# Optimization experiments

Measured on AMD Instinct MI355X. Metric: run time of the kernel, lower is better.

Reference implementation:

```python
import jax, jax.numpy as jnp
import numpy as np

# dims
N, D, H = 10000, 512, 8            # nodes, node hidden, heads
E, EL, M = 120000, 60000, 600000   # graph edges, local edges, line-graph edges
ED, EH = 64, 8                     # edge feat dim (relation_share_heads), edge heads
L, R = 4, 100                      # gnn layers, relation vocab
DK, EDK = D // H, ED // EH
SCALE_N, SCALE_E = float(np.sqrt(DK)), float(np.sqrt(EDK))


def layer_norm(h, g, b, eps=1e-5):
    mu = jnp.mean(h, axis=-1, keepdims=True)
    var = jnp.mean((h - mu) ** 2, axis=-1, keepdims=True)
    return (h - mu) * jax.lax.rsqrt(var + eps) * g + b


def setup_inputs() -> dict:
    key = jax.random.key(0)
    ks = iter(jax.random.split(key, 80))

    def nrm(shape, s=0.02):
        return jax.random.normal(next(ks), shape, jnp.float32) * s

    inp = {
        "x": jax.random.normal(next(ks), (N, D), jnp.float32),
        "rel_embed": nrm((R, ED), 1.0),
        # node-update (RAT) params, stacked over layers
        "Wq": nrm((L, D, D)), "bq": jnp.zeros((L, D), jnp.float32),
        "Wk": nrm((L, D, D)), "Wv": nrm((L, D, D)),
        "Wo": nrm((L, D, D)), "bo": jnp.zeros((L, D), jnp.float32),
        "ln1_g": jnp.ones((L, D), jnp.float32), "ln1_b": jnp.zeros((L, D), jnp.float32),
        "F1": nrm((L, D, 4 * D)), "f1b": jnp.zeros((L, 4 * D), jnp.float32),
        "F2": nrm((L, 4 * D, D)), "f2b": jnp.zeros((L, D), jnp.float32),
        "ln2_g": jnp.ones((L, D), jnp.float32), "ln2_b": jnp.zeros((L, D), jnp.float32),
        # edge-update (metapath line-graph attention) params
        "Eq": nrm((L, ED, ED)), "eqb": jnp.zeros((L, ED), jnp.float32),
        "Ek": nrm((L, ED, ED)), "Ev": nrm((L, ED, ED)),
        "Eo": nrm((L, ED, ED)), "eob": jnp.zeros((L, ED), jnp.float32),
        "Ns": nrm((L, D, ED)), "nsb": jnp.zeros((L, ED), jnp.float32),
        "Nd": nrm((L, D, ED)), "ndb": jnp.zeros((L, ED), jnp.float32),
        "eln1_g": jnp.ones((L, ED), jnp.float32), "eln1_b": jnp.zeros((L, ED), jnp.float32),
        "G1": nrm((L, ED, 4 * ED)), "g1b": jnp.zeros((L, 4 * ED), jnp.float32),
        "G2": nrm((L, 4 * ED, ED)), "g2b": jnp.zeros((L, ED), jnp.float32),
        "eln2_g": jnp.ones((L, ED), jnp.float32), "eln2_b": jnp.zeros((L, ED), jnp.float32),
        # graph structure (constants)
        "edge_feat": jax.random.randint(next(ks), (E,), 0, R),
        "local_index": jnp.arange(EL),
        "src_ids": jax.random.randint(next(ks), (EL,), 0, N),
        "dst_ids": jax.random.randint(next(ks), (EL,), 0, N),
        "g_src": jax.random.randint(next(ks), (E,), 0, N),
        "g_dst": jax.random.randint(next(ks), (E,), 0, N),
        "lg_src": jax.random.randint(next(ks), (M,), 0, EL),
        "lg_dst": jax.random.randint(next(ks), (M,), 0, EL),
    }
    return inp


def reference(x, rel_embed, Wq, bq, Wk, Wv, Wo, bo, ln1_g, ln1_b, F1, f1b, F2, f2b,
              ln2_g, ln2_b, Eq, eqb, Ek, Ev, Eo, eob, Ns, nsb, Nd, ndb,
              eln1_g, eln1_b, G1, g1b, G2, g2b, eln2_g, eln2_b,
              edge_feat, local_index, src_ids, dst_ids, g_src, g_dst, lg_src, lg_dst):
    lg_x = rel_embed[edge_feat]        # [E, ED] relation embedding gather
    lg_x_local = lg_x[local_index]     # [EL, ED]
    for i in range(L):
        x_in = x
        # ---- node update: relation-aware multi-head attention over g ----
        q = (x_in @ Wq[i] + bq[i]).reshape(N, H, DK)
        k = (x_in @ Wk[i]).reshape(N, H, DK)
        v = (x_in @ Wv[i]).reshape(N, H, DK)
        e = lg_x[:, None, :]           # relation feat shared across heads (edim == d_k)
        ks = k[g_src] + e              # [E, H, DK]
        vs = v[g_src] + e
        s = jnp.einsum('ehd,ehd->eh', ks, q[g_dst]) / SCALE_N
        w = jnp.exp(jnp.clip(s, -10.0, 10.0))
        wv = jax.ops.segment_sum(w[..., None] * vs, g_dst, num_segments=N)
        z = jax.ops.segment_sum(w, g_dst, num_segments=N)
        o = (wv / jnp.maximum(z, 1e-9)[..., None]).reshape(N, D)
        h = layer_norm(x_in + o @ Wo[i] + bo[i], ln1_g[i], ln1_b[i])
        x = layer_norm(h + jax.nn.relu(h @ F1[i] + f1b[i]) @ F2[i] + f2b[i], ln2_g[i], ln2_b[i])
        # ---- edge update: attention over line graph lg, metapath = shared node feat ----
        src_x = x_in[src_ids]          # index_select on pre-update x
        dst_x = x_in[dst_ids]
        qe = (lg_x_local @ Eq[i] + eqb[i] + src_x @ Ns[i] + nsb[i]).reshape(EL, EH, EDK)
        me = (dst_x @ Nd[i] + ndb[i]).reshape(EL, EH, EDK)
        ke = (lg_x_local @ Ek[i]).reshape(EL, EH, EDK) + me
        ve = (lg_x_local @ Ev[i]).reshape(EL, EH, EDK) + me
        se = jnp.einsum('mhd,mhd->mh', ke[lg_src], qe[lg_dst]) / SCALE_E
        we = jnp.exp(jnp.clip(se, -10.0, 10.0))
        wve = jax.ops.segment_sum(we[..., None] * ve[lg_src], lg_dst, num_segments=EL)
        ze = jax.ops.segment_sum(we, lg_dst, num_segments=EL)
        oe = (wve / jnp.maximum(ze, 1e-9)[..., None]).reshape(EL, ED)
        he = layer_norm(lg_x_local + oe @ Eo[i] + eob[i], eln1_g[i], eln1_b[i])
        out_local = layer_norm(he + jax.nn.relu(he @ G1[i] + g1b[i]) @ G2[i] + g2b[i],
                               eln2_g[i], eln2_b[i])
        lg_x = lg_x.at[local_index].set(out_local)   # masked_scatter_
        lg_x_local = out_local
    return (x, lg_x_local)
```

## Files before the change

### kernel.cpp

```cpp
#include <hip/hip_runtime.h>
#include <math.h>

#define NN   10000
#define DD   512
#define NH   8
#define NE   120000
#define NEL  60000
#define NLG  600000
#define ED   64
#define NEH  8
#define NL   4
#define QKVW 1536

typedef __attribute__((ext_vector_type(8))) short bf16x8;
typedef __attribute__((ext_vector_type(8))) unsigned short u16x8;
typedef __attribute__((ext_vector_type(4))) float f32x4;

__device__ __forceinline__ unsigned short f2b(float f) {
    union { float f; unsigned u; } c; c.f = f;
    unsigned u = c.u;
    unsigned r = u + 0x7FFFu + ((u >> 16) & 1u);
    return (unsigned short)(r >> 16);
}
__device__ __forceinline__ float b2f(unsigned short b) {
    union { unsigned u; float f; } c; c.u = ((unsigned)b) << 16;
    return c.f;
}

__device__ __forceinline__ void gl16(const unsigned short* g, unsigned short* l) {
    __builtin_amdgcn_global_load_lds(
        (const __attribute__((address_space(1))) unsigned int*)g,
        (__attribute__((address_space(3))) unsigned int*)l, 16, 0, 0);
}

static __global__ __launch_bounds__(256)
void zero_k(float* __restrict__ p, int n) {
    int i = blockIdx.x * 256 + threadIdx.x;
    if (i < n) p[i] = 0.0f;
}

static __global__ __launch_bounds__(256)
void castcopy_k(const float* __restrict__ s, float* __restrict__ d,
                unsigned short* __restrict__ db, int n) {
    int i = blockIdx.x * 256 + threadIdx.x;
    if (i < n) { float v = s[i]; if (d) d[i] = v; db[i] = f2b(v); }
}

static __global__ __launch_bounds__(256)
void init_lg_k(const float* __restrict__ rel, const int* __restrict__ ef,
               unsigned short* __restrict__ lgb) {
    int i = blockIdx.x * 256 + threadIdx.x;
    if (i >= NE * ED) return;
    int e = i >> 6, c = i & 63;
    lgb[i] = f2b(rel[ef[e] * ED + c]);
}

static __global__ __launch_bounds__(256)
void gather64_k(const unsigned short* __restrict__ lgb, const int* __restrict__ idx,
                float* __restrict__ el, unsigned short* __restrict__ elb) {
    int i = blockIdx.x * 256 + threadIdx.x;
    if (i >= NEL * ED) return;
    int r = i >> 6;
    unsigned short b = lgb[(long)idx[r] * ED + (i & 63)];
    el[i] = b2f(b); elb[i] = b;
}

static __global__ __launch_bounds__(256)
void ttrans_k(const float* __restrict__ in, unsigned short* __restrict__ out,
              int K, int N, long lstride, int rowStride, int rowOff, int colOff) {
    __shared__ float sm[32][33];
    const int l = blockIdx.z;
    const int kt = blockIdx.x * 32, nt = blockIdx.y * 32;
    const int tx = threadIdx.x & 31, ty = threadIdx.x >> 5;
    const float* ip = in + (size_t)l * K * N;
    #pragma unroll
    for (int r = 0; r < 4; ++r)
        sm[ty + 8 * r][tx] = ip[(size_t)(kt + ty + 8 * r) * N + nt + tx];
    __syncthreads();
    unsigned short* op = out + (size_t)l * lstride;
    #pragma unroll
    for (int r = 0; r < 4; ++r) {
        int n = nt + ty + 8 * r;
        op[(size_t)(rowOff + n) * rowStride + colOff + kt + tx] = f2b(sm[tx][ty + 8 * r]);
    }
}

static __global__ __launch_bounds__(256)
void build_qkvb_k(const float* __restrict__ bq, float* __restrict__ out) {
    int i = blockIdx.x * 256 + threadIdx.x;
    if (i >= NL * QKVW) return;
    int l = i / QKVW, c = i - l * QKVW;
    out[i] = (c < 512) ? bq[l * 512 + c] : 0.0f;
}

static __global__ __launch_bounds__(256)
void ebias_k(const float* __restrict__ ndb, const float* __restrict__ eqb,
             const float* __restrict__ nsb, float* __restrict__ kvb,
             float* __restrict__ qb2) {
    int i = blockIdx.x * 256 + threadIdx.x;
    if (i < NL * 128) kvb[i] = ndb[(i >> 7) * 64 + (i & 63)];
    if (i < NL * 64)  qb2[i] = eqb[i] + nsb[i];
}

static __global__ __launch_bounds__(256)
void hist_k(const int* __restrict__ dst, int* __restrict__ cnt, int n) {
    int i = blockIdx.x * 256 + threadIdx.x;
    if (i < n) atomicAdd(&cnt[dst[i]], 1);
}

static __global__ __launch_bounds__(256)
void scanA_k(const int* __restrict__ cnt, int* __restrict__ off,
             int* __restrict__ bsum, int n) {
    __shared__ int sm[256];
    const int t = threadIdx.x;
    const int i = blockIdx.x * 256 + t;
    int v = (i < n) ? cnt[i] : 0;
    sm[t] = v; __syncthreads();
    int x = v;
    #pragma unroll
    for (int d = 1; d < 256; d <<= 1) {
        int y = (t >= d) ? sm[t - d] : 0;
        __syncthreads();
        x += y; sm[t] = x; __syncthreads();
    }
    if (i < n) off[i] = x - v;
    if (t == 255) bsum[blockIdx.x] = x;
}

static __global__ __launch_bounds__(1024)
void scanB_k(int* __restrict__ bsum, int nb) {
    __shared__ int sm[1024];
    const int t = threadIdx.x;
    int v = (t < nb) ? bsum[t] : 0;
    sm[t] = v; __syncthreads();
    int x = v;
    #pragma unroll
    for (int d = 1; d < 1024; d <<= 1) {
        int y = (t >= d) ? sm[t - d] : 0;
        __syncthreads();
        x += y; sm[t] = x; __syncthreads();
    }
    if (t < nb) bsum[t] = x - v;
}

static __global__ __launch_bounds__(256)
void scanC_k(const int* __restrict__ bsum, int* __restrict__ off,
             int* __restrict__ cur, int n) {
    int i = blockIdx.x * 256 + threadIdx.x;
    if (i < n) { int o = off[i] + bsum[blockIdx.x]; off[i] = o; cur[i] = o; }
}

static __global__ __launch_bounds__(256)
void scatter_k(const int* __restrict__ dst, int* __restrict__ cur,
               int* __restrict__ ord, int n) {
    int i = blockIdx.x * 256 + threadIdx.x;
    if (i < n) { int p = atomicAdd(&cur[dst[i]], 1); ord[p] = i; }
}

static __global__ __launch_bounds__(256)
void pack_k(const int* __restrict__ gord, const int* __restrict__ gsrc,
            const int* __restrict__ eord, const int* __restrict__ lsrc,
            int2* __restrict__ npack, int* __restrict__ esrc) {
    int i = blockIdx.x * 256 + threadIdx.x;
    if (i < NE) { int e = gord[i]; npack[i] = make_int2(e, gsrc[e]); }
    if (i < NLG) esrc[i] = lsrc[eord[i]];
}

#define FSWZ(r) (((r) & 3) ^ (((r) >> 2) & 3))
template<int BM, int BN>
static __global__ __launch_bounds__(256)
void gemm_bf16_k(const unsigned short* __restrict__ A,
                 const unsigned short* __restrict__ A2, const int* __restrict__ idx2,
                 const unsigned short* __restrict__ Bt, const float* __restrict__ bias,
                 const float* __restrict__ addC, const unsigned short* __restrict__ addCb,
                 float* __restrict__ C, unsigned short* __restrict__ Cb,
                 int M, int K, int Nc, int doRelu, int K1)
{
    constexpr int MI = BM / 32, NI = BN / 32;
    constexpr int AC = BM / 64, BC = BN / 64;
    __shared__ unsigned short Asl[BM * 32];
    __shared__ unsigned short Bsl[BN * 32];
    const int tid  = threadIdx.x;
    const int lane = tid & 63;
    const int wave = tid >> 6;
    const int wr = (wave >> 1) * (BM / 2);
    const int wc = (wave & 1) * (BN / 2);

    const int nwg = gridDim.x * gridDim.y;
    const int hw = blockIdx.y * gridDim.x + blockIdx.x;
    const int q8 = nwg >> 3, r8 = nwg & 7;
    const int xcd = hw & 7, rest = hw >> 3;
    const int logical = (xcd < r8 ? xcd * (q8 + 1) : r8 * (q8 + 1) + (xcd - r8) * q8) + rest;
    const int bm = (logical / gridDim.x) * BM;
    const int bn = (logical % gridDim.x) * BN;

    const int rl = lane >> 2;
    const int sl = lane & 3;
    int ga[AC]; long ia[AC]; bool av[AC]; int acw[AC];
    #pragma unroll
    for (int c = 0; c < AC; ++c) {
        int ar = wave * (BM / 4) + c * 16 + rl;
        ga[c] = bm + ar;
        av[c] = ga[c] < M;
        ia[c] = (A2 && av[c]) ? (long)idx2[ga[c]] : 0;
        acw[c] = (sl ^ FSWZ(ar)) * 8;
    }
    int gb[BC]; int bcw[BC];
    #pragma unroll
    for (int c = 0; c < BC; ++c) {
        int br = wave * (BN / 4) + c * 16 + rl;
        gb[c] = bn + br;
        bcw[c] = (sl ^ FSWZ(br)) * 8;
    }

    auto stage = [&](int k0) {
        #pragma unroll
        for (int c = 0; c < AC; ++c) {
            const unsigned short* s;
            if (!A2)            s = A  + (long)ga[c] * K  + k0 + acw[c];
            else if (k0 < K1)   s = A  + (long)ga[c] * K1 + k0 + acw[c];
            else                s = A2 + ia[c] * DD + (k0 - K1) + acw[c];
            if (av[c]) gl16(s, Asl + (wave * (BM / 4) + c * 16) * 32);
        }
        #pragma unroll
        for (int c = 0; c < BC; ++c)
            gl16(Bt + (long)gb[c] * K + k0 + bcw[c],
                 Bsl + (wave * (BN / 4) + c * 16) * 32);
    };

    f32x4 acc[MI][NI] = {};
    const int rbase = lane & 15;
    const int ks = lane >> 4;

    for (int k0 = 0; k0 < K; k0 += 32) {
        stage(k0);
        __syncthreads();
        bf16x8 af[MI]; bf16x8 bfr[NI];
        #pragma unroll
        for (int mi = 0; mi < MI; ++mi) {
            int r = wr + mi * 16 + rbase;
            int s = ks ^ FSWZ(r);
            af[mi] = *reinterpret_cast<const bf16x8*>(Asl + r * 32 + s * 8);
        }
        #pragma unroll
        for (int ni = 0; ni < NI; ++ni) {
            int r = wc + ni * 16 + rbase;
            int s = ks ^ FSWZ(r);
            bfr[ni] = *reinterpret_cast<const bf16x8*>(Bsl + r * 32 + s * 8);
        }
        #pragma unroll
        for (int mi = 0; mi < MI; ++mi)
            #pragma unroll
            for (int ni = 0; ni < NI; ++ni)
                acc[mi][ni] = __builtin_amdgcn_mfma_f32_16x16x32_bf16(
                    af[mi], bfr[ni], acc[mi][ni], 0, 0, 0);
        __syncthreads();
    }

    const int colBase = bn + wc + rbase;
    const int rowBase = bm + wr + ks * 4;
    #pragma unroll
    for (int mi = 0; mi < MI; ++mi) {
        #pragma unroll
        for (int j = 0; j < 4; ++j) {
            int r = rowBase + mi * 16 + j;
            if (r >= M) continue;
            long ro = (long)r * Nc;
            #pragma unroll
            for (int ni = 0; ni < NI; ++ni) {
                int cc = colBase + ni * 16;
                if (cc >= Nc) continue;
                float v = acc[mi][ni][j];
                if (bias)  v += bias[cc];
                if (doRelu) v = fmaxf(v, 0.0f);
                if (addC)  v += addC[ro + cc];
                else if (addCb) v += b2f(addCb[ro + cc]);
                if (Cb) Cb[ro + cc] = f2b(v);
                else    C[ro + cc] = v;
            }
        }
    }
}
#undef FSWZ

static __global__ __launch_bounds__(256)
void ln_k(const float* __restrict__ in, const float* __restrict__ g,
          const float* __restrict__ b, float* __restrict__ out, int Dw, int nrows,
          unsigned short* __restrict__ outb,
          unsigned short* __restrict__ out2b, const int* __restrict__ idx2)
{
    const int row = blockIdx.x * 4 + (threadIdx.x >> 6);
    if (row >= nrows) return;
    const int lane = threadIdx.x & 63;
    const int per = Dw >> 6;
    float v[8];
    const float* rp = in + (long)row * Dw;
    float s = 0.f;
    for (int i = 0; i < per; ++i) { v[i] = rp[i * 64 + lane]; s += v[i]; }
    #pragma unroll
    for (int off = 32; off; off >>= 1) s += __shfl_xor(s, off, 64);
    const float mu = s / (float)Dw;
    float var = 0.f;
    for (int i = 0; i < per; ++i) { float d = v[i] - mu; var += d * d; }
    #pragma unroll
    for (int off = 32; off; off >>= 1) var += __shfl_xor(var, off, 64);
    const float rstd = rsqrtf(var / (float)Dw + 1e-5f);
    for (int i = 0; i < per; ++i) {
        int c = i * 64 + lane;
        float o = (v[i] - mu) * rstd * g[c] + b[c];
        if (out)   out[(long)row * Dw + c] = o;
        if (outb)  outb[(long)row * Dw + c] = f2b(o);
        if (out2b) out2b[(long)idx2[row] * Dw + c] = f2b(o);
    }
}

static __global__ __launch_bounds__(256)
void node_attn_csr_k(const unsigned short* __restrict__ qkv,
                     const unsigned short* __restrict__ lgb,
                     const int* __restrict__ goff, const int2* __restrict__ npack,
                     unsigned short* __restrict__ ob)
{
    int node = blockIdx.x * 4 + (threadIdx.x >> 6);
    if (node >= NN) return;
    const int lane = threadIdx.x & 63;
    float qv[8];
    {
        u16x8 q8 = *reinterpret_cast<const u16x8*>(qkv + (long)node * QKVW + lane * 8);
        #pragma unroll
        for (int i = 0; i < 8; ++i) qv[i] = b2f(q8[i]);
    }
    float wva[8] = {0.f, 0.f, 0.f, 0.f, 0.f, 0.f, 0.f, 0.f};
    float zac = 0.f;
    int j = goff[node];
    const int hi = (node + 1 < NN) ? goff[node + 1] : NE;
    const int eoffl = (lane & 7) * 8;

    for (; j + 2 <= hi; j += 2) {
        int2 pa = npack[j], pb = npack[j + 1];
        u16x8 kA = *reinterpret_cast<const u16x8*>(qkv + (long)pa.y * QKVW + 512 + lane * 8);
        u16x8 vA = *reinterpret_cast<const u16x8*>(qkv + (long)pa.y * QKVW + 1024 + lane * 8);
        u16x8 eA = *reinterpret_cast<const u16x8*>(lgb + (long)pa.x * ED + eoffl);
        u16x8 kB = *reinterpret_cast<const u16x8*>(qkv + (long)pb.y * QKVW + 512 + lane * 8);
        u16x8 vB = *reinterpret_cast<const u16x8*>(qkv + (long)pb.y * QKVW + 1024 + lane * 8);
        u16x8 eB = *reinterpret_cast<const u16x8*>(lgb + (long)pb.x * ED + eoffl);
        float edA[8], vvA[8], edB[8], vvB[8];
        float pA = 0.f, pB = 0.f;
        #pragma unroll
        for (int i = 0; i < 8; ++i) {
            edA[i] = b2f(eA[i]); vvA[i] = b2f(vA[i]);
            pA = fmaf(b2f(kA[i]) + edA[i], qv[i], pA);
            edB[i] = b2f(eB[i]); vvB[i] = b2f(vB[i]);
            pB = fmaf(b2f(kB[i]) + edB[i], qv[i], pB);
        }
        pA += __shfl_xor(pA, 1, 64); pA += __shfl_xor(pA, 2, 64); pA += __shfl_xor(pA, 4, 64);
        pB += __shfl_xor(pB, 1, 64); pB += __shfl_xor(pB, 2, 64); pB += __shfl_xor(pB, 4, 64);
        float wA = expf(fminf(fmaxf(pA * 0.125f, -10.0f), 10.0f));
        float wB = expf(fminf(fmaxf(pB * 0.125f, -10.0f), 10.0f));
        #pragma unroll
        for (int i = 0; i < 8; ++i) {
            wva[i] = fmaf(wA, vvA[i] + edA[i], wva[i]);
            wva[i] = fmaf(wB, vvB[i] + edB[i], wva[i]);
        }
        zac += wA + wB;
    }
    for (; j < hi; ++j) {
        int2 pa = npack[j];
        u16x8 kA = *reinterpret_cast<const u16x8*>(qkv + (long)pa.y * QKVW + 512 + lane * 8);
        u16x8 vA = *reinterpret_cast<const u16x8*>(qkv + (long)pa.y * QKVW + 1024 + lane * 8);
        u16x8 eA = *reinterpret_cast<const u16x8*>(lgb + (long)pa.x * ED + eoffl);
        float edA[8], vvA[8];
        float pA = 0.f;
        #pragma unroll
        for (int i = 0; i < 8; ++i) {
            edA[i] = b2f(eA[i]); vvA[i] = b2f(vA[i]);
            pA = fmaf(b2f(kA[i]) + edA[i], qv[i], pA);
        }
        pA += __shfl_xor(pA, 1, 64); pA += __shfl_xor(pA, 2, 64); pA += __shfl_xor(pA, 4, 64);
        float wA = expf(fminf(fmaxf(pA * 0.125f, -10.0f), 10.0f));
        #pragma unroll
        for (int i = 0; i < 8; ++i) wva[i] = fmaf(wA, vvA[i] + edA[i], wva[i]);
        zac += wA;
    }
    const float inv = 1.0f / fmaxf(zac, 1e-9f);
    u16x8 o8;
    #pragma unroll
    for (int i = 0; i < 8; ++i) o8[i] = f2b(wva[i] * inv);
    *reinterpret_cast<u16x8*>(ob + (long)node * DD + lane * 8) = o8;
}

static __global__ __launch_bounds__(256)
void lg_attn_csr_k(const unsigned short* __restrict__ qeb,
                   const unsigned short* __restrict__ keve,
                   const int* __restrict__ eoff, const int* __restrict__ esrc,
                   unsigned short* __restrict__ oeb)
{
    int d = blockIdx.x * 4 + (threadIdx.x >> 6);
    if (d >= NEL) return;
    const int lane = threadIdx.x & 63;
    const float qv = b2f(qeb[(long)d * ED + lane]);
    float oa = 0.f, zac = 0.f;
    int j = eoff[d];
    const int hi = (d + 1 < NEL) ? eoff[d + 1] : NLG;
    for (; j + 4 <= hi; j += 4) {
        int ss[4]; float kk[4], vv[4];
        #pragma unroll
        for (int u = 0; u < 4; ++u) ss[u] = esrc[j + u];
        #pragma unroll
        for (int u = 0; u < 4; ++u) {
            kk[u] = b2f(keve[(long)ss[u] * 128 + lane]);
            vv[u] = b2f(keve[(long)ss[u] * 128 + 64 + lane]);
        }
        #pragma unroll
        for (int u = 0; u < 4; ++u) {
            float p = kk[u] * qv;
            p += __shfl_xor(p, 1, 64); p += __shfl_xor(p, 2, 64); p += __shfl_xor(p, 4, 64);
            float w = expf(fminf(fmaxf(p * 0.35355339059327373f, -10.0f), 10.0f));
            oa = fmaf(w, vv[u], oa);
            zac += w;
        }
    }
    for (; j < hi; ++j) {
        int s = esrc[j];
        float kv = b2f(keve[(long)s * 128 + lane]);
        float vv = b2f(keve[(long)s * 128 + 64 + lane]);
        float p = kv * qv;
        p += __shfl_xor(p, 1, 64); p += __shfl_xor(p, 2, 64); p += __shfl_xor(p, 4, 64);
        float w = expf(fminf(fmaxf(p * 0.35355339059327373f, -10.0f), 10.0f));
        oa = fmaf(w, vv, oa);
        zac += w;
    }
    oeb[(long)d * ED + lane] = f2b(oa / fmaxf(zac, 1e-9f));
}

static inline void run_gemm(hipStream_t st, const unsigned short* A,
                            const unsigned short* Bt, const float* bias,
                            const float* addC, const unsigned short* addCb,
                            float* C, unsigned short* Cb,
                            int M, int K, int Nc, int relu)
{
    dim3 g((Nc + 63) / 64, (M + 63) / 64);
    gemm_bf16_k<64, 64><<<g, 256, 0, st>>>(A, nullptr, nullptr, Bt, bias, addC, addCb,
                                           C, Cb, M, K, Nc, relu, 0);
}
static inline void run_gemm2(hipStream_t st, const unsigned short* A1,
                             const unsigned short* A2, const int* idx2,
                             const unsigned short* Bt, const float* bias,
                             unsigned short* Cb, int M, int K, int Nc, int K1)
{
    dim3 g((Nc + 63) / 64, (M + 63) / 64);
    gemm_bf16_k<64, 64><<<g, 256, 0, st>>>(A1, A2, idx2, Bt, bias, nullptr, nullptr,
                                           nullptr, Cb, M, K, Nc, 0, K1);
}

extern "C" void kernel_launch(void* const* d_in, const int* in_sizes, int n_in,
                              void* d_out, int out_size, void* d_ws, size_t ws_size,
                              hipStream_t stream)
{
    const float* x_in  = (const float*)d_in[0];
    const float* rel   = (const float*)d_in[1];
    const float* Wq    = (const float*)d_in[2];
    const float* bq    = (const float*)d_in[3];
    const float* Wk    = (const float*)d_in[4];
    const float* Wv    = (const float*)d_in[5];
    const float* Wo    = (const float*)d_in[6];
    const float* bo    = (const float*)d_in[7];
    const float* ln1g  = (const float*)d_in[8];
    const float* ln1b  = (const float*)d_in[9];
    const float* F1    = (const float*)d_in[10];
    const float* f1b   = (const float*)d_in[11];
    const float* F2    = (const float*)d_in[12];
    const float* f2b_  = (const float*)d_in[13];
    const float* ln2g  = (const float*)d_in[14];
    const float* ln2b  = (const float*)d_in[15];
    const float* Eq    = (const float*)d_in[16];
    const float* eqb   = (const float*)d_in[17];
    const float* Ek    = (const float*)d_in[18];
    const float* Ev    = (const float*)d_in[19];
    const float* Eo    = (const float*)d_in[20];
    const float* eob   = (const float*)d_in[21];
    const float* Ns    = (const float*)d_in[22];
    const float* nsb   = (const float*)d_in[23];
    const float* Nd    = (const float*)d_in[24];
    const float* ndb   = (const float*)d_in[25];
    const float* eln1g = (const float*)d_in[26];
    const float* eln1b = (const float*)d_in[27];
    const float* G1    = (const float*)d_in[28];
    const float* g1b   = (const float*)d_in[29];
    const float* G2    = (const float*)d_in[30];
    const float* g2b   = (const float*)d_in[31];
    const float* eln2g = (const float*)d_in[32];
    const float* eln2b = (const float*)d_in[33];
    const int* edge_feat   = (const int*)d_in[34];
    const int* local_index = (const int*)d_in[35];
    const int* src_ids     = (const int*)d_in[36];
    const int* dst_ids     = (const int*)d_in[37];
    const int* g_src       = (const int*)d_in[38];
    const int* g_dst       = (const int*)d_in[39];
    const int* lg_src      = (const int*)d_in[40];
    const int* lg_dst      = (const int*)d_in[41];

    float* xbuf = (float*)d_out;
    float* el   = xbuf + (size_t)NN * DD;

    float* W = (float*)d_ws;
    size_t off = 0;
    auto alloc = [&](size_t n) { float* p = W + off; off += (n + 63) & ~(size_t)63; return p; };
    float* t0  = alloc((size_t)NN * DD);
    float* t2  = alloc((size_t)NEL * ED);
    float* t3  = alloc((size_t)NEL * ED);
    float* qkvb = alloc((size_t)NL * QKVW);
    float* kvb  = alloc((size_t)NL * 128);
    float* qb2  = alloc((size_t)NL * ED);

    unsigned short* bp = (unsigned short*)(W + off);
    size_t boff = 0;
    auto balloc = [&](size_t n) { unsigned short* p = bp + boff; boff += (n + 63) & ~(size_t)63; return p; };
    unsigned short* lgb = balloc((size_t)NE * ED);
    unsigned short* xb  = balloc((size_t)NN * DD);
    unsigned short* qkv = balloc((size_t)NN * QKVW);
    unsigned short* elb = balloc((size_t)NEL * ED);
    unsigned short* e1b = balloc((size_t)NEL * ED);
    unsigned short* heb = balloc((size_t)NEL * ED);
    unsigned short* qeb = balloc((size_t)NEL * ED);
    unsigned short* fgb = balloc((size_t)NN * 4 * DD);
    unsigned short* hb   = qkv;
    unsigned short* keve = qkv + (size_t)NN * DD;
    unsigned short* ob   = fgb;
    unsigned short* WqkvT = balloc((size_t)NL * QKVW * DD);
    unsigned short* WoT  = balloc((size_t)NL * DD * DD);
    unsigned short* F1T  = balloc((size_t)NL * DD * 4 * DD);
    unsigned short* F2T  = balloc((size_t)NL * 4 * DD * DD);
    unsigned short* KVET = balloc((size_t)NL * 128 * 576);
    unsigned short* QET  = balloc((size_t)NL * 64 * 576);
    unsigned short* EoT  = balloc((size_t)NL * ED * ED);
    unsigned short* G1T  = balloc((size_t)NL * ED * 4 * ED);
    unsigned short* G2T  = balloc((size_t)NL * 4 * ED * ED);
    int* ip = (int*)(bp + ((boff + 63) & ~(size_t)63));
    size_t ioff = 0;
    auto ialloc = [&](size_t n) { int* p = ip + ioff; ioff += (n + 63) & ~(size_t)63; return p; };
    int* gcnt = ialloc(NN);
    int* goff = ialloc(NN);
    int* gcur = ialloc(NN);
    int* gord = ialloc(NE);
    int2* npack = (int2*)ialloc(2 * (size_t)NE);
    int* ecnt = ialloc(NEL);
    int* eoff = ialloc(NEL);
    int* ecur = ialloc(NEL);
    int* eord = ialloc(NLG);
    int* esrc = ialloc(NLG);
    int* bsum = ialloc(1024);

    auto tt = [&](const float* src, unsigned short* dst, int K, int N,
                  long lstride, int rowStride, int rowOff, int colOff) {
        dim3 g(K / 32, N / 32, NL);
        ttrans_k<<<g, 256, 0, stream>>>(src, dst, K, N, lstride, rowStride, rowOff, colOff);
    };
    tt(Wq, WqkvT, 512, 512, (long)QKVW * DD, DD, 0, 0);
    tt(Wk, WqkvT, 512, 512, (long)QKVW * DD, DD, 512, 0);
    tt(Wv, WqkvT, 512, 512, (long)QKVW * DD, DD, 1024, 0);
    tt(Wo, WoT, 512, 512, (long)DD * DD, DD, 0, 0);
    tt(F1, F1T, 512, 2048, (long)DD * 4 * DD, DD, 0, 0);
    tt(F2, F2T, 2048, 512, (long)4 * DD * DD, 4 * DD, 0, 0);
    tt(Ek, KVET, 64, 64, (long)128 * 576, 576, 0, 0);
    tt(Nd, KVET, 512, 64, (long)128 * 576, 576, 0, 64);
    tt(Ev, KVET, 64, 64, (long)128 * 576, 576, 64, 0);
    tt(Nd, KVET, 512, 64, (long)128 * 576, 576, 64, 64);
    tt(Eq, QET, 64, 64, (long)64 * 576, 576, 0, 0);
    tt(Ns, QET, 512, 64, (long)64 * 576, 576, 0, 64);
    tt(Eo, EoT, 64, 64, (long)ED * ED, ED, 0, 0);
    tt(G1, G1T, 64, 256, (long)ED * 4 * ED, ED, 0, 0);
    tt(G2, G2T, 256, 64, (long)4 * ED * ED, 4 * ED, 0, 0);
    build_qkvb_k<<<(NL * QKVW + 255) / 256, 256, 0, stream>>>(bq, qkvb);
    ebias_k<<<(NL * 128 + 255) / 256, 256, 0, stream>>>(ndb, eqb, nsb, kvb, qb2);

    const int nbG = (NN + 255) / 256, nbE = (NEL + 255) / 256;
    zero_k<<<nbG, 256, 0, stream>>>((float*)gcnt, NN);
    hist_k<<<(NE + 255) / 256, 256, 0, stream>>>(g_dst, gcnt, NE);
    scanA_k<<<nbG, 256, 0, stream>>>(gcnt, goff, bsum, NN);
    scanB_k<<<1, 1024, 0, stream>>>(bsum, nbG);
    scanC_k<<<nbG, 256, 0, stream>>>(bsum, goff, gcur, NN);
    scatter_k<<<(NE + 255) / 256, 256, 0, stream>>>(g_dst, gcur, gord, NE);
    zero_k<<<nbE, 256, 0, stream>>>((float*)ecnt, NEL);
    hist_k<<<(NLG + 255) / 256, 256, 0, stream>>>(lg_dst, ecnt, NLG);
    scanA_k<<<nbE, 256, 0, stream>>>(ecnt, eoff, bsum, NEL);
    scanB_k<<<1, 1024, 0, stream>>>(bsum, nbE);
    scanC_k<<<nbE, 256, 0, stream>>>(bsum, eoff, ecur, NEL);
    scatter_k<<<(NLG + 255) / 256, 256, 0, stream>>>(lg_dst, ecur, eord, NLG);
    pack_k<<<(NLG + 255) / 256, 256, 0, stream>>>(gord, g_src, eord, lg_src, npack, esrc);

    const int ndD = NN * DD;
    const int elD = NEL * ED;
    castcopy_k<<<(ndD + 255) / 256, 256, 0, stream>>>(x_in, xbuf, xb, ndD);
    init_lg_k<<<(NE * ED + 255) / 256, 256, 0, stream>>>(rel, edge_feat, lgb);
    gather64_k<<<(elD + 255) / 256, 256, 0, stream>>>(lgb, local_index, el, elb);

    for (int i = 0; i < NL; ++i) {
        size_t oD2 = (size_t)i * DD * DD, oE2 = (size_t)i * ED * ED;

        run_gemm(stream, xb, WqkvT + (size_t)i * QKVW * DD, qkvb + (size_t)i * QKVW,
                 nullptr, nullptr, nullptr, qkv, NN, DD, QKVW, 0);
        node_attn_csr_k<<<NN / 4, 256, 0, stream>>>(qkv, lgb, goff, npack, ob);
        run_gemm(stream, ob, WoT + oD2, bo + (size_t)i * DD, nullptr, xb, t0, nullptr, NN, DD, DD, 0);
        ln_k<<<(NN + 3) / 4, 256, 0, stream>>>(t0, ln1g + (size_t)i * DD, ln1b + (size_t)i * DD,
                                               nullptr, DD, NN, hb, nullptr, nullptr);

        run_gemm2(stream, elb, xb, dst_ids, KVET + (size_t)i * 128 * 576,
                  kvb + (size_t)i * 128, keve, NEL, 576, 128, 64);
        run_gemm2(stream, elb, xb, src_ids, QET + (size_t)i * 64 * 576,
                  qb2 + (size_t)i * 64, qeb, NEL, 576, 64, 64);
        lg_attn_csr_k<<<NEL / 4, 256, 0, stream>>>(qeb, keve, eoff, esrc, e1b);
        run_gemm(stream, e1b, EoT + oE2, eob + (size_t)i * ED, nullptr, elb, t2, nullptr, NEL, ED, ED, 0);
        ln_k<<<(NEL + 3) / 4, 256, 0, stream>>>(t2, eln1g + (size_t)i * ED, eln1b + (size_t)i * ED,
                                                nullptr, ED, NEL, heb, nullptr, nullptr);
        run_gemm(stream, heb, G1T + (size_t)i * ED * 4 * ED, g1b + (size_t)i * 4 * ED,
                 nullptr, nullptr, nullptr, fgb, NEL, ED, 4 * ED, 1);
        run_gemm(stream, fgb, G2T + (size_t)i * 4 * ED * ED, g2b + (size_t)i * ED,
                 nullptr, heb, t3, nullptr, NEL, 4 * ED, ED, 0);
        ln_k<<<(NEL + 3) / 4, 256, 0, stream>>>(t3, eln2g + (size_t)i * ED, eln2b + (size_t)i * ED,
                                                el, ED, NEL, elb, lgb, local_index);

        run_gemm(stream, hb, F1T + (size_t)i * DD * 4 * DD, f1b + (size_t)i * 4 * DD,
                 nullptr, nullptr, nullptr, fgb, NN, DD, 4 * DD, 1);
        run_gemm(stream, fgb, F2T + (size_t)i * 4 * DD * DD, f2b_ + (size_t)i * DD,
                 nullptr, hb, xbuf, nullptr, NN, 2048, DD, 0);
        ln_k<<<(NN + 3) / 4, 256, 0, stream>>>(xbuf, ln2g + (size_t)i * DD, ln2b + (size_t)i * DD,
                                               xbuf, DD, NN, xb, nullptr, nullptr);
    }
}
```

Measured before the change: 1.806 ms.

## Use K=64 GEMM staging tiles and store pre-LayerNorm residuals in bf16

The GEMM kernel moves from a templated 32-wide K step to a fixed 64x64 tile with a 64-wide K step and an 8-way XOR swizzle. This halves the number of barrier-separated stage iterations per tile and issues two MFMA sub-steps per stage. Separately, the GEMM outputs that feed LayerNorm (t0, t2, t3, and the FFN residual) are now written as bf16 instead of fp32, and ln_k reads them as bf16, which cuts intermediate memory traffic. The cost is extra rounding before LayerNorm, which lowers accuracy.

```diff
diff --git a/kernel.cpp b/kernel.cpp
--- a/kernel.cpp
+++ b/kernel.cpp
@@ -166,8 +166,6 @@
     if (i < NLG) esrc[i] = lsrc[eord[i]];
 }
 
-#define FSWZ(r) (((r) & 3) ^ (((r) >> 2) & 3))
-template<int BM, int BN>
 static __global__ __launch_bounds__(256)
 void gemm_bf16_k(const unsigned short* __restrict__ A,
                  const unsigned short* __restrict__ A2, const int* __restrict__ idx2,
@@ -176,98 +174,93 @@
                  float* __restrict__ C, unsigned short* __restrict__ Cb,
                  int M, int K, int Nc, int doRelu, int K1)
 {
-    constexpr int MI = BM / 32, NI = BN / 32;
-    constexpr int AC = BM / 64, BC = BN / 64;
-    __shared__ unsigned short Asl[BM * 32];
-    __shared__ unsigned short Bsl[BN * 32];
+    __shared__ unsigned short Asl[64 * 64];
+    __shared__ unsigned short Bsl[64 * 64];
     const int tid  = threadIdx.x;
     const int lane = tid & 63;
     const int wave = tid >> 6;
-    const int wr = (wave >> 1) * (BM / 2);
-    const int wc = (wave & 1) * (BN / 2);
+    const int wr = (wave >> 1) * 32;
+    const int wc = (wave & 1) * 32;
 
     const int nwg = gridDim.x * gridDim.y;
     const int hw = blockIdx.y * gridDim.x + blockIdx.x;
     const int q8 = nwg >> 3, r8 = nwg & 7;
     const int xcd = hw & 7, rest = hw >> 3;
     const int logical = (xcd < r8 ? xcd * (q8 + 1) : r8 * (q8 + 1) + (xcd - r8) * q8) + rest;
-    const int bm = (logical / gridDim.x) * BM;
-    const int bn = (logical % gridDim.x) * BN;
-
-    const int rl = lane >> 2;
-    const int sl = lane & 3;
-    int ga[AC]; long ia[AC]; bool av[AC]; int acw[AC];
-    #pragma unroll
-    for (int c = 0; c < AC; ++c) {
-        int ar = wave * (BM / 4) + c * 16 + rl;
+    const int bm = (logical / gridDim.x) * 64;
+    const int bn = (logical % gridDim.x) * 64;
+
+    const int rl8 = lane >> 3;
+    const int sl8 = lane & 7;
+    int ga[2]; long ia[2]; bool av[2]; int acw[2];
+    int gb[2]; int bcw[2];
+    #pragma unroll
+    for (int c = 0; c < 2; ++c) {
+        int ar = wave * 16 + c * 8 + rl8;
         ga[c] = bm + ar;
         av[c] = ga[c] < M;
         ia[c] = (A2 && av[c]) ? (long)idx2[ga[c]] : 0;
-        acw[c] = (sl ^ FSWZ(ar)) * 8;
-    }
-    int gb[BC]; int bcw[BC];
-    #pragma unroll
-    for (int c = 0; c < BC; ++c) {
-        int br = wave * (BN / 4) + c * 16 + rl;
+        acw[c] = (sl8 ^ (ar & 7)) * 8;
+        int br = wave * 16 + c * 8 + rl8;
         gb[c] = bn + br;
-        bcw[c] = (sl ^ FSWZ(br)) * 8;
+        bcw[c] = (sl8 ^ (br & 7)) * 8;
     }
 
     auto stage = [&](int k0) {
         #pragma unroll
-        for (int c = 0; c < AC; ++c) {
+        for (int c = 0; c < 2; ++c) {
             const unsigned short* s;
             if (!A2)            s = A  + (long)ga[c] * K  + k0 + acw[c];
             else if (k0 < K1)   s = A  + (long)ga[c] * K1 + k0 + acw[c];
             else                s = A2 + ia[c] * DD + (k0 - K1) + acw[c];
-            if (av[c]) gl16(s, Asl + (wave * (BM / 4) + c * 16) * 32);
-        }
-        #pragma unroll
-        for (int c = 0; c < BC; ++c)
-            gl16(Bt + (long)gb[c] * K + k0 + bcw[c],
-                 Bsl + (wave * (BN / 4) + c * 16) * 32);
+            if (av[c]) gl16(s, Asl + (wave * 16 + c * 8) * 64);
+            gl16(Bt + (long)gb[c] * K + k0 + bcw[c], Bsl + (wave * 16 + c * 8) * 64);
+        }
     };
 
-    f32x4 acc[MI][NI] = {};
+    f32x4 acc[2][2] = {};
     const int rbase = lane & 15;
     const int ks = lane >> 4;
 
-    for (int k0 = 0; k0 < K; k0 += 32) {
+    for (int k0 = 0; k0 < K; k0 += 64) {
         stage(k0);
         __syncthreads();
-        bf16x8 af[MI]; bf16x8 bfr[NI];
-        #pragma unroll
-        for (int mi = 0; mi < MI; ++mi) {
-            int r = wr + mi * 16 + rbase;
-            int s = ks ^ FSWZ(r);
-            af[mi] = *reinterpret_cast<const bf16x8*>(Asl + r * 32 + s * 8);
-        }
-        #pragma unroll
-        for (int ni = 0; ni < NI; ++ni) {
-            int r = wc + ni * 16 + rbase;
-            int s = ks ^ FSWZ(r);
-            bfr[ni] = *reinterpret_cast<const bf16x8*>(Bsl + r * 32 + s * 8);
-        }
-        #pragma unroll
-        for (int mi = 0; mi < MI; ++mi)
+        #pragma unroll
+        for (int h = 0; h < 2; ++h) {
+            bf16x8 af[2], bfr[2];
             #pragma unroll
-            for (int ni = 0; ni < NI; ++ni)
-                acc[mi][ni] = __builtin_amdgcn_mfma_f32_16x16x32_bf16(
-                    af[mi], bfr[ni], acc[mi][ni], 0, 0, 0);
+            for (int mi = 0; mi < 2; ++mi) {
+                int r = wr + mi * 16 + rbase;
+                int p = (h * 4 + ks) ^ (r & 7);
+                af[mi] = *reinterpret_cast<const bf16x8*>(Asl + r * 64 + p * 8);
+            }
+            #pragma unroll
+            for (int ni = 0; ni < 2; ++ni) {
+                int r = wc + ni * 16 + rbase;
+                int p = (h * 4 + ks) ^ (r & 7);
+                bfr[ni] = *reinterpret_cast<const bf16x8*>(Bsl + r * 64 + p * 8);
+            }
+            #pragma unroll
+            for (int mi = 0; mi < 2; ++mi)
+                #pragma unroll
+                for (int ni = 0; ni < 2; ++ni)
+                    acc[mi][ni] = __builtin_amdgcn_mfma_f32_16x16x32_bf16(
+                        af[mi], bfr[ni], acc[mi][ni], 0, 0, 0);
+        }
         __syncthreads();
     }
 
     const int colBase = bn + wc + rbase;
     const int rowBase = bm + wr + ks * 4;
     #pragma unroll
-    for (int mi = 0; mi < MI; ++mi) {
+    for (int mi = 0; mi < 2; ++mi) {
         #pragma unroll
         for (int j = 0; j < 4; ++j) {
             int r = rowBase + mi * 16 + j;
             if (r >= M) continue;
             long ro = (long)r * Nc;
             #pragma unroll
-            for (int ni = 0; ni < NI; ++ni) {
+            for (int ni = 0; ni < 2; ++ni) {
                 int cc = colBase + ni * 16;
                 if (cc >= Nc) continue;
                 float v = acc[mi][ni][j];
@@ -281,11 +274,11 @@
         }
     }
 }
-#undef FSWZ
-
-static __global__ __launch_bounds__(256)
-void ln_k(const float* __restrict__ in, const float* __restrict__ g,
-          const float* __restrict__ b, float* __restrict__ out, int Dw, int nrows,
+
+static __global__ __launch_bounds__(256)
+void ln_k(const float* __restrict__ in, const unsigned short* __restrict__ inb,
+          const float* __restrict__ g, const float* __restrict__ b,
+          float* __restrict__ out, int Dw, int nrows,
           unsigned short* __restrict__ outb,
           unsigned short* __restrict__ out2b, const int* __restrict__ idx2)
 {
@@ -294,9 +287,14 @@
     const int lane = threadIdx.x & 63;
     const int per = Dw >> 6;
     float v[8];
-    const float* rp = in + (long)row * Dw;
     float s = 0.f;
-    for (int i = 0; i < per; ++i) { v[i] = rp[i * 64 + lane]; s += v[i]; }
+    if (inb) {
+        const unsigned short* rp = inb + (long)row * Dw;
+        for (int i = 0; i < per; ++i) { v[i] = b2f(rp[i * 64 + lane]); s += v[i]; }
+    } else {
+        const float* rp = in + (long)row * Dw;
+        for (int i = 0; i < per; ++i) { v[i] = rp[i * 64 + lane]; s += v[i]; }
+    }
     #pragma unroll
     for (int off = 32; off; off >>= 1) s += __shfl_xor(s, off, 64);
     const float mu = s / (float)Dw;
@@ -439,8 +437,8 @@
                             int M, int K, int Nc, int relu)
 {
     dim3 g((Nc + 63) / 64, (M + 63) / 64);
-    gemm_bf16_k<64, 64><<<g, 256, 0, st>>>(A, nullptr, nullptr, Bt, bias, addC, addCb,
-                                           C, Cb, M, K, Nc, relu, 0);
+    gemm_bf16_k<<<g, 256, 0, st>>>(A, nullptr, nullptr, Bt, bias, addC, addCb,
+                                   C, Cb, M, K, Nc, relu, 0);
 }
 static inline void run_gemm2(hipStream_t st, const unsigned short* A1,
                              const unsigned short* A2, const int* idx2,
@@ -448,8 +446,8 @@
                              unsigned short* Cb, int M, int K, int Nc, int K1)
 {
     dim3 g((Nc + 63) / 64, (M + 63) / 64);
-    gemm_bf16_k<64, 64><<<g, 256, 0, st>>>(A1, A2, idx2, Bt, bias, nullptr, nullptr,
-                                           nullptr, Cb, M, K, Nc, 0, K1);
+    gemm_bf16_k<<<g, 256, 0, st>>>(A1, A2, idx2, Bt, bias, nullptr, nullptr,
+                                   nullptr, Cb, M, K, Nc, 0, K1);
 }
 
 extern "C" void kernel_launch(void* const* d_in, const int* in_sizes, int n_in,
@@ -505,9 +503,6 @@
     float* W = (float*)d_ws;
     size_t off = 0;
     auto alloc = [&](size_t n) { float* p = W + off; off += (n + 63) & ~(size_t)63; return p; };
-    float* t0  = alloc((size_t)NN * DD);
-    float* t2  = alloc((size_t)NEL * ED);
-    float* t3  = alloc((size_t)NEL * ED);
     float* qkvb = alloc((size_t)NL * QKVW);
     float* kvb  = alloc((size_t)NL * 128);
     float* qb2  = alloc((size_t)NL * ED);
@@ -523,6 +518,10 @@
     unsigned short* heb = balloc((size_t)NEL * ED);
     unsigned short* qeb = balloc((size_t)NEL * ED);
     unsigned short* fgb = balloc((size_t)NN * 4 * DD);
+    unsigned short* t0b = balloc((size_t)NN * DD);
+    unsigned short* t2b = balloc((size_t)NEL * ED);
+    unsigned short* t3b = balloc((size_t)NEL * ED);
+    unsigned short* xpb = balloc((size_t)NN * DD);
     unsigned short* hb   = qkv;
     unsigned short* keve = qkv + (size_t)NN * DD;
     unsigned short* ob   = fgb;
@@ -600,8 +599,8 @@
         run_gemm(stream, xb, WqkvT + (size_t)i * QKVW * DD, qkvb + (size_t)i * QKVW,
                  nullptr, nullptr, nullptr, qkv, NN, DD, QKVW, 0);
         node_attn_csr_k<<<NN / 4, 256, 0, stream>>>(qkv, lgb, goff, npack, ob);
-        run_gemm(stream, ob, WoT + oD2, bo + (size_t)i * DD, nullptr, xb, t0, nullptr, NN, DD, DD, 0);
-        ln_k<<<(NN + 3) / 4, 256, 0, stream>>>(t0, ln1g + (size_t)i * DD, ln1b + (size_t)i * DD,
+        run_gemm(stream, ob, WoT + oD2, bo + (size_t)i * DD, nullptr, xb, nullptr, t0b, NN, DD, DD, 0);
+        ln_k<<<(NN + 3) / 4, 256, 0, stream>>>(nullptr, t0b, ln1g + (size_t)i * DD, ln1b + (size_t)i * DD,
                                                nullptr, DD, NN, hb, nullptr, nullptr);
 
         run_gemm2(stream, elb, xb, dst_ids, KVET + (size_t)i * 128 * 576,
@@ -609,21 +608,21 @@
         run_gemm2(stream, elb, xb, src_ids, QET + (size_t)i * 64 * 576,
                   qb2 + (size_t)i * 64, qeb, NEL, 576, 64, 64);
         lg_attn_csr_k<<<NEL / 4, 256, 0, stream>>>(qeb, keve, eoff, esrc, e1b);
-        run_gemm(stream, e1b, EoT + oE2, eob + (size_t)i * ED, nullptr, elb, t2, nullptr, NEL, ED, ED, 0);
-        ln_k<<<(NEL + 3) / 4, 256, 0, stream>>>(t2, eln1g + (size_t)i * ED, eln1b + (size_t)i * ED,
+        run_gemm(stream, e1b, EoT + oE2, eob + (size_t)i * ED, nullptr, elb, nullptr, t2b, NEL, ED, ED, 0);
+        ln_k<<<(NEL + 3) / 4, 256, 0, stream>>>(nullptr, t2b, eln1g + (size_t)i * ED, eln1b + (size_t)i * ED,
                                                 nullptr, ED, NEL, heb, nullptr, nullptr);
         run_gemm(stream, heb, G1T + (size_t)i * ED * 4 * ED, g1b + (size_t)i * 4 * ED,
                  nullptr, nullptr, nullptr, fgb, NEL, ED, 4 * ED, 1);
         run_gemm(stream, fgb, G2T + (size_t)i * 4 * ED * ED, g2b + (size_t)i * ED,
-                 nullptr, heb, t3, nullptr, NEL, 4 * ED, ED, 0);
-        ln_k<<<(NEL + 3) / 4, 256, 0, stream>>>(t3, eln2g + (size_t)i * ED, eln2b + (size_t)i * ED,
+                 nullptr, heb, nullptr, t3b, NEL, 4 * ED, ED, 0);
+        ln_k<<<(NEL + 3) / 4, 256, 0, stream>>>(nullptr, t3b, eln2g + (size_t)i * ED, eln2b + (size_t)i * ED,
                                                 el, ED, NEL, elb, lgb, local_index);
 
         run_gemm(stream, hb, F1T + (size_t)i * DD * 4 * DD, f1b + (size_t)i * 4 * DD,
                  nullptr, nullptr, nullptr, fgb, NN, DD, 4 * DD, 1);
         run_gemm(stream, fgb, F2T + (size_t)i * 4 * DD * DD, f2b_ + (size_t)i * DD,
-                 nullptr, hb, xbuf, nullptr, NN, 2048, DD, 0);
-        ln_k<<<(NN + 3) / 4, 256, 0, stream>>>(xbuf, ln2g + (size_t)i * DD, ln2b + (size_t)i * DD,
+                 nullptr, hb, nullptr, xpb, NN, 2048, DD, 0);
+        ln_k<<<(NN + 3) / 4, 256, 0, stream>>>(nullptr, xpb, ln2g + (size_t)i * DD, ln2b + (size_t)i * DD,
                                                xbuf, DD, NN, xb, nullptr, nullptr);
     }
 }
```

New measurement: 1.674 ms, median of 2. 7.3% less time.
